# Kernel optimization log

Hardware: AMD Instinct MI355X
Metric: run time of the kernel (lower is better)

The kernel has to match this reference:

```python
import jax, jax.numpy as jnp
import numpy as np

EMBED_DIM = 1024
NUM_HEADS = 16
HEAD_DIM = EMBED_DIM // NUM_HEADS


def setup_inputs() -> dict:
    key = jax.random.key(0)
    k1, k2, k3 = jax.random.split(key, 3)
    B, S = 2, 2048
    scale_in = 1.0 / np.sqrt(EMBED_DIM)
    x = jax.random.normal(k1, (B, S, EMBED_DIM), dtype=jnp.float32)
    Wqkv = jax.random.normal(k2, (EMBED_DIM, 3 * EMBED_DIM), dtype=jnp.float32) * scale_in
    bqkv = jnp.zeros((3 * EMBED_DIM,), dtype=jnp.float32)
    Wout = jax.random.normal(k3, (EMBED_DIM, EMBED_DIM), dtype=jnp.float32) * scale_in
    bout = jnp.zeros((EMBED_DIM,), dtype=jnp.float32)
    return {"x": x, "Wqkv": Wqkv, "bqkv": bqkv, "Wout": Wout, "bout": bout}


def reference(x, Wqkv, bqkv, Wout, bout):
    # Causal multi-head self-attention (dropout in eval mode = identity).
    B, S, E = x.shape
    qkv = x @ Wqkv + bqkv                                  # [B,S,3E]
    qkv = qkv.reshape(B, S, 3, NUM_HEADS, HEAD_DIM)
    qkv = jnp.transpose(qkv, (2, 0, 3, 1, 4))              # [3,B,H,S,D]
    q, k, v = qkv[0], qkv[1], qkv[2]
    scores = jnp.einsum("bhqd,bhkd->bhqk", q, k) / np.sqrt(HEAD_DIM)
    causal = jnp.tril(jnp.ones((S, S), dtype=bool))
    scores = jnp.where(causal, scores, -jnp.inf)
    attn = jax.nn.softmax(scores, axis=-1)                 # [B,H,S,S]
    out = jnp.einsum("bhqk,bhkd->bhqd", attn, v)           # [B,H,S,D]
    out = jnp.transpose(out, (0, 2, 1, 3)).reshape(B, S, E)
    return out @ Wout + bout
```

## Files before the change

kernel.cpp:

```cpp
#include <hip/hip_runtime.h>
#include <hip/hip_bf16.h>

#define BB 2
#define SS 2048
#define EE 1024
#define HH 16
#define DD 64
#define MT (BB*SS)
#define NQ (3*EE)

typedef unsigned short u16;
typedef __bf16 bf16t;
typedef bf16t bf16x8 __attribute__((ext_vector_type(8)));
typedef short short8v __attribute__((ext_vector_type(8)));
typedef float f32x4 __attribute__((ext_vector_type(4)));

#define AS1 __attribute__((address_space(1)))
#define AS3 __attribute__((address_space(3)))

__device__ __forceinline__ u16 f2b(float f) {
  unsigned u = __builtin_bit_cast(unsigned, f);
  u += 0x7FFF + ((u >> 16) & 1);
  return (u16)(u >> 16);
}

__device__ __forceinline__ unsigned cvtpk(float lo, float hi) {
  unsigned r;
  asm("v_cvt_pk_bf16_f32 %0, %1, %2" : "=v"(r) : "v"(lo), "v"(hi));
  return r;
}

__device__ __forceinline__ void gload_lds16(const void* g, void* l) {
  __builtin_amdgcn_global_load_lds((const AS1 void*)(g), (AS3 void*)(l), 16, 0, 0);
}

__device__ __forceinline__ f32x4 mfma_bf16(short8v a, short8v b, f32x4 c) {
  return __builtin_amdgcn_mfma_f32_16x16x32_bf16(
      __builtin_bit_cast(bf16x8, a), __builtin_bit_cast(bf16x8, b), c, 0, 0, 0);
}

#define QSCALE 0.18033688f

__global__ void __launch_bounds__(256) cast_kernel(const float* __restrict__ in,
                                                   u16* __restrict__ out, int n) {
  int i = (blockIdx.x * 256 + threadIdx.x) * 4;
  if (i + 3 < n) {
    float4 v = *(const float4*)(in + i);
    ushort4 o;
    o.x = f2b(v.x); o.y = f2b(v.y); o.z = f2b(v.z); o.w = f2b(v.w);
    *(ushort4*)(out + i) = o;
  }
}

__global__ void __launch_bounds__(256) transpose_kernel(const float* __restrict__ W,
                                                        u16* __restrict__ WT,
                                                        int K, int N) {
  __shared__ float t[64][65];
  int k0 = blockIdx.y * 64, n0 = blockIdx.x * 64;
  int r = threadIdx.x >> 4;
  int c4 = (threadIdx.x & 15) * 4;
#pragma unroll
  for (int i = 0; i < 4; ++i) {
    float4 v = *(const float4*)(W + (size_t)(k0 + r + i * 16) * N + n0 + c4);
    t[r + i * 16][c4 + 0] = v.x; t[r + i * 16][c4 + 1] = v.y;
    t[r + i * 16][c4 + 2] = v.z; t[r + i * 16][c4 + 3] = v.w;
  }
  __syncthreads();
#pragma unroll
  for (int i = 0; i < 4; ++i) {
    ushort4 o;
    o.x = f2b(t[c4 + 0][r + i * 16]); o.y = f2b(t[c4 + 1][r + i * 16]);
    o.z = f2b(t[c4 + 2][r + i * 16]); o.w = f2b(t[c4 + 3][r + i * 16]);
    *(ushort4*)(WT + (size_t)(n0 + r + i * 16) * K + k0 + c4) = o;
  }
}

__global__ void __launch_bounds__(256) gemm_qkv_kernel(
    const u16* __restrict__ A, const u16* __restrict__ BT,
    const float* __restrict__ bias,
    u16* __restrict__ Qs, u16* __restrict__ Ks, u16* __restrict__ Vt) {
  __shared__ u16 As[8192];
  __shared__ u16 Bs[8192];
  const int K = EE;
  int tid = threadIdx.x;
  int w = tid >> 6, lane = tid & 63;
  int g = lane >> 4, q = lane & 15;
  int m0 = blockIdx.y * 128, n0 = blockIdx.x * 128;
  int wm = (w >> 1) * 64, wn = (w & 1) * 64;

  f32x4 acc[4][4] = {};

  int r = tid >> 2;
  int kc = (tid & 3) * 8;
  const u16* ga = A + (size_t)(m0 + r) * K + kc;
  const u16* gb = BT + (size_t)(n0 + r) * K + kc;
  u16* lA0 = As + w * 512;
  u16* lA1 = As + 2048 + w * 512;
  u16* lB0 = Bs + w * 512;
  u16* lB1 = Bs + 2048 + w * 512;

  gload_lds16(ga, lA0);
  gload_lds16(ga + 64 * K, lA1);
  gload_lds16(gb, lB0);
  gload_lds16(gb + 64 * K, lB1);
  ga += 32; gb += 32;
  __syncthreads();

  int cur = 0;
  for (int k0 = 0; k0 < K; k0 += 32) {
    if (k0 + 32 < K) {
      int nx = (cur ^ 1) * 4096;
      gload_lds16(ga, lA0 + nx);
      gload_lds16(ga + 64 * K, lA1 + nx);
      gload_lds16(gb, lB0 + nx);
      gload_lds16(gb + 64 * K, lB1 + nx);
      ga += 32; gb += 32;
    }
    const u16* Ab = As + cur * 4096;
    const u16* Bb = Bs + cur * 4096;
    short8v af[4], bfv[4];
#pragma unroll
    for (int m = 0; m < 4; ++m)
      af[m] = *(const short8v*)(Ab + (wm + m * 16 + q) * 32 + g * 8);
#pragma unroll
    for (int n = 0; n < 4; ++n)
      bfv[n] = *(const short8v*)(Bb + (wn + n * 16 + q) * 32 + g * 8);
#pragma unroll
    for (int m = 0; m < 4; ++m)
#pragma unroll
      for (int n = 0; n < 4; ++n)
        acc[m][n] = mfma_bf16(af[m], bfv[n], acc[m][n]);
    __syncthreads();
    cur ^= 1;
  }

#pragma unroll
  for (int m = 0; m < 4; ++m) {
    int row0 = m0 + wm + m * 16 + g * 4;
#pragma unroll
    for (int n = 0; n < 4; ++n) {
      int col = n0 + wn + n * 16 + q;
      float bi = bias[col];
      int t = col >> 10;
      int h = (col >> 6) & 15;
      int d = col & 63;
      int b = row0 >> 11, s0 = row0 & 2047;
      size_t bh = (size_t)b * HH + h;
      if (t == 2) {
        ushort4 vv;
        vv.x = f2b(acc[m][n][0] + bi); vv.y = f2b(acc[m][n][1] + bi);
        vv.z = f2b(acc[m][n][2] + bi); vv.w = f2b(acc[m][n][3] + bi);
        *(ushort4*)&Vt[(bh * DD + d) * SS + s0] = vv;
      } else if (t == 0) {
#pragma unroll
        for (int r2 = 0; r2 < 4; ++r2)
          Qs[(bh * SS + s0 + r2) * DD + d] = f2b((acc[m][n][r2] + bi) * QSCALE);
      } else {
#pragma unroll
        for (int r2 = 0; r2 < 4; ++r2)
          Ks[(bh * SS + s0 + r2) * DD + d] = f2b(acc[m][n][r2] + bi);
      }
    }
  }
}

__global__ void __launch_bounds__(512) attn_kernel(
    const u16* __restrict__ Qg, const u16* __restrict__ Kg,
    const u16* __restrict__ Vg, u16* __restrict__ O) {
  __shared__ char lds[49152];
  const int tid = threadIdx.x;
  const int w = tid >> 6, lane = tid & 63;
  const int g = lane >> 4, q = lane & 15;
  const int bid = blockIdx.x;
  const int bh = bid & 31;
  const int p = 15 - (bid >> 5);
  const int b = bh >> 4, h = bh & 15;
  char* Pw = lds + 32768 + w * 2048;
  const int qsw = (q & 7) << 4;

  const char* Qp = (const char*)Qg + (size_t)bh * (SS * 128);
  const char* Kp = (const char*)Kg + (size_t)bh * (SS * 128);
  const char* Vp = (const char*)Vg + (size_t)bh * (SS * 128);

  const int srow = tid >> 3;
  const int ssw = ((tid & 7) * 16) ^ ((srow & 7) << 4);
  const char* Ksrc = Kp + srow * 128 + ssw;
  const char* Vsrc = Vp + (size_t)srow * (SS * 2) + ssw;
  char* Kdst = lds + w * 1024;
  char* Vdst = lds + 16384 + w * 1024;

  const int nt = 2 * p + 2;
  const int qw = p * 128 + w * 16;

  short8v aq0 = *(const short8v*)(Qp + (size_t)(qw + q) * 128 + g * 16);
  short8v aq1 = *(const short8v*)(Qp + (size_t)(qw + q) * 128 + 64 + g * 16);

  f32x4 oacc[4] = {};
  float mrun = -1e30f, lrun = 0.f;

  gload_lds16(Ksrc, Kdst);
  gload_lds16(Vsrc, Vdst);
  __syncthreads();

  for (int s = 0; s < nt; ++s) {
    const int buf = s & 1;
    if (s + 1 < nt) {
      gload_lds16(Ksrc + (size_t)(s + 1) * 8192, Kdst + (buf ^ 1) * 8192);
      gload_lds16(Vsrc + (s + 1) * 128, Vdst + (buf ^ 1) * 8192);
    }
    const int kv0 = s << 6;
    if (kv0 <= qw + 15) {
      const char* Kc = lds + buf * 8192;
      const char* Vc = lds + 16384 + buf * 8192;
      short8v kf[4][2];
#pragma unroll
      for (int cc = 0; cc < 4; ++cc) {
        const char* kb = Kc + (cc * 16 + q) * 128;
        kf[cc][0] = *(const short8v*)(kb + ((g * 16) ^ qsw));
        kf[cc][1] = *(const short8v*)(kb + ((64 + g * 16) ^ qsw));
      }
      f32x4 st[4];
#pragma unroll
      for (int cc = 0; cc < 4; ++cc) {
        f32x4 z = {};
        z = mfma_bf16(kf[cc][0], aq0, z);
        z = mfma_bf16(kf[cc][1], aq1, z);
        st[cc] = z;
      }
      short8v vf[4][2];
#pragma unroll
      for (int v = 0; v < 4; ++v) {
        const char* vb = Vc + (v * 16 + q) * 128;
        vf[v][0] = *(const short8v*)(vb + ((g * 16) ^ qsw));
        vf[v][1] = *(const short8v*)(vb + ((64 + g * 16) ^ qsw));
      }
      if (kv0 + 63 > qw) {
        int row = qw + q;
#pragma unroll
        for (int cc = 0; cc < 4; ++cc) {
          int kvb = kv0 + cc * 16 + g * 4;
#pragma unroll
          for (int r2 = 0; r2 < 4; ++r2)
            if (kvb + r2 > row) st[cc][r2] = -1e30f;
        }
      }
      f32x4 t01, t23;
#pragma unroll
      for (int r2 = 0; r2 < 4; ++r2) {
        t01[r2] = fmaxf(st[0][r2], st[1][r2]);
        t23[r2] = fmaxf(st[2][r2], st[3][r2]);
      }
      float mx = fmaxf(fmaxf(fmaxf(t01[0], t01[1]), fmaxf(t01[2], t01[3])),
                       fmaxf(fmaxf(t23[0], t23[1]), fmaxf(t23[2], t23[3])));
      mx = fmaxf(mx, __shfl_xor(mx, 16));
      mx = fmaxf(mx, __shfl_xor(mx, 32));
      if (!__all(mx - mrun <= 8.f)) {
        float mnew = fmaxf(mrun, mx);
        float alpha = exp2f(mrun - mnew);
        mrun = mnew;
        lrun *= alpha;
#pragma unroll
        for (int vfi = 0; vfi < 4; ++vfi)
#pragma unroll
          for (int r2 = 0; r2 < 4; ++r2) oacc[vfi][r2] *= alpha;
      }
      f32x4 sum4 = {};
#pragma unroll
      for (int cc = 0; cc < 4; ++cc)
#pragma unroll
        for (int r2 = 0; r2 < 4; ++r2) {
          float pv = exp2f(st[cc][r2] - mrun);
          st[cc][r2] = pv;
          sum4[r2] += pv;
        }
      float sm = (sum4[0] + sum4[1]) + (sum4[2] + sum4[3]);
      sm += __shfl_xor(sm, 16);
      sm += __shfl_xor(sm, 32);
      lrun += sm;
      char* basep = Pw + q * 128;
#pragma unroll
      for (int cc = 0; cc < 4; ++cc) {
        unsigned p01 = cvtpk(st[cc][0], st[cc][1]);
        unsigned p23 = cvtpk(st[cc][2], st[cc][3]);
        *(unsigned*)(basep + ((32 * cc + 8 * g + 0) ^ qsw)) = p01;
        *(unsigned*)(basep + ((32 * cc + 8 * g + 4) ^ qsw)) = p23;
      }
      short8v pa0 = *(const short8v*)(basep + ((g * 16) ^ qsw));
      short8v pa1 = *(const short8v*)(basep + ((64 + g * 16) ^ qsw));
#pragma unroll
      for (int vfi = 0; vfi < 4; ++vfi) {
        oacc[vfi] = mfma_bf16(vf[vfi][0], pa0, oacc[vfi]);
        oacc[vfi] = mfma_bf16(vf[vfi][1], pa1, oacc[vfi]);
      }
    }
    __syncthreads();
  }

  {
    float inv = 1.0f / lrun;
    int row = qw + q;
    char* obase = (char*)O + (((size_t)b * SS + row) * EE + h * 64) * 2;
#pragma unroll
    for (int vfi = 0; vfi < 4; ++vfi) {
      uint2 o;
      o.x = cvtpk(oacc[vfi][0] * inv, oacc[vfi][1] * inv);
      o.y = cvtpk(oacc[vfi][2] * inv, oacc[vfi][3] * inv);
      *(uint2*)(obase + (vfi * 16 + g * 4) * 2) = o;
    }
  }
}

__global__ void __launch_bounds__(256) gemm_out_kernel(
    const u16* __restrict__ A, const u16* __restrict__ BT,
    const float* __restrict__ bias, float* __restrict__ Cout) {
  __shared__ u16 As[8192];
  __shared__ u16 Bs[8192];
  const int K = EE;
  int tid = threadIdx.x;
  int w = tid >> 6, lane = tid & 63;
  int g = lane >> 4, q = lane & 15;
  int m0 = blockIdx.y * 128, n0 = blockIdx.x * 128;
  int wm = (w >> 1) * 64, wn = (w & 1) * 64;

  f32x4 acc[4][4] = {};

  int r = tid >> 2;
  int kc = (tid & 3) * 8;
  const u16* ga = A + (size_t)(m0 + r) * K + kc;
  const u16* gb = BT + (size_t)(n0 + r) * K + kc;
  u16* lA0 = As + w * 512;
  u16* lA1 = As + 2048 + w * 512;
  u16* lB0 = Bs + w * 512;
  u16* lB1 = Bs + 2048 + w * 512;

  gload_lds16(ga, lA0);
  gload_lds16(ga + 64 * K, lA1);
  gload_lds16(gb, lB0);
  gload_lds16(gb + 64 * K, lB1);
  ga += 32; gb += 32;
  __syncthreads();

  int cur = 0;
  for (int k0 = 0; k0 < K; k0 += 32) {
    if (k0 + 32 < K) {
      int nx = (cur ^ 1) * 4096;
      gload_lds16(ga, lA0 + nx);
      gload_lds16(ga + 64 * K, lA1 + nx);
      gload_lds16(gb, lB0 + nx);
      gload_lds16(gb + 64 * K, lB1 + nx);
      ga += 32; gb += 32;
    }
    const u16* Ab = As + cur * 4096;
    const u16* Bb = Bs + cur * 4096;
    short8v af[4], bfv[4];
#pragma unroll
    for (int m = 0; m < 4; ++m)
      af[m] = *(const short8v*)(Ab + (wm + m * 16 + q) * 32 + g * 8);
#pragma unroll
    for (int n = 0; n < 4; ++n)
      bfv[n] = *(const short8v*)(Bb + (wn + n * 16 + q) * 32 + g * 8);
#pragma unroll
    for (int m = 0; m < 4; ++m)
#pragma unroll
      for (int n = 0; n < 4; ++n)
        acc[m][n] = mfma_bf16(af[m], bfv[n], acc[m][n]);
    __syncthreads();
    cur ^= 1;
  }

#pragma unroll
  for (int m = 0; m < 4; ++m) {
    int row0 = m0 + wm + m * 16 + g * 4;
#pragma unroll
    for (int n = 0; n < 4; ++n) {
      int col = n0 + wn + n * 16 + q;
      float bi = bias[col];
#pragma unroll
      for (int r2 = 0; r2 < 4; ++r2) {
        int row = row0 + r2;
        Cout[(size_t)row * EE + col] = acc[m][n][r2] + bi;
      }
    }
  }
}

extern "C" void kernel_launch(void* const* d_in, const int* in_sizes, int n_in,
                              void* d_out, int out_size, void* d_ws, size_t ws_size,
                              hipStream_t stream) {
  (void)in_sizes; (void)n_in; (void)out_size; (void)ws_size;
  const float* x    = (const float*)d_in[0];
  const float* Wqkv = (const float*)d_in[1];
  const float* bqkv = (const float*)d_in[2];
  const float* Wout = (const float*)d_in[3];
  const float* bout = (const float*)d_in[4];
  float* out = (float*)d_out;

  char* p = (char*)d_ws;
  u16* xb  = (u16*)p; p += (size_t)MT * EE * 2;
  u16* wqT = (u16*)p; p += (size_t)NQ * EE * 2;
  u16* woT = (u16*)p; p += (size_t)EE * EE * 2;
  u16* Qs  = (u16*)p; p += (size_t)BB * HH * SS * DD * 2;
  u16* Ks  = (u16*)p; p += (size_t)BB * HH * SS * DD * 2;
  u16* Vt  = (u16*)p; p += (size_t)BB * HH * DD * SS * 2;
  u16* Ob  = (u16*)p; p += (size_t)MT * EE * 2;

  cast_kernel<<<dim3((MT * EE / 4) / 256), dim3(256), 0, stream>>>(x, xb, MT * EE);
  transpose_kernel<<<dim3(NQ / 64, EE / 64), dim3(256), 0, stream>>>(Wqkv, wqT, EE, NQ);
  transpose_kernel<<<dim3(EE / 64, EE / 64), dim3(256), 0, stream>>>(Wout, woT, EE, EE);
  gemm_qkv_kernel<<<dim3(NQ / 128, MT / 128), dim3(256), 0, stream>>>(xb, wqT, bqkv, Qs, Ks, Vt);
  attn_kernel<<<dim3(512), dim3(512), 0, stream>>>(Qs, Ks, Vt, Ob);
  gemm_out_kernel<<<dim3(EE / 128, MT / 128), dim3(256), 0, stream>>>(Ob, woT, bout, out);
}
```

Baseline: 121.1 us.

## Split attention into 64-row query blocks with snake ordering and MFMA priority

The attention kernel moves from 512 blocks of 8 waves (128 query rows each) to 1024 blocks of 4 waves (64 query rows each). Each thread now issues two K and two V LDS loads per tile to fill the same 64-row tile, and LDS shrinks to 40 KB. Causal blocks are ordered in a serpentine pattern so consecutive blocks get balanced work. s_setprio brackets around the MFMA loops raise wave priority during matrix ops. The intent is better occupancy and load balance across CUs, at the cost of more blocks each reloading K/V with less reuse per block.

Result: slower. 126.5 us (+4.5%).

```diff
diff --git a/kernel.cpp b/kernel.cpp
--- a/kernel.cpp
+++ b/kernel.cpp
@@ -164,16 +164,18 @@
   }
 }
 
-__global__ void __launch_bounds__(512) attn_kernel(
+__global__ void __launch_bounds__(256) attn_kernel(
     const u16* __restrict__ Qg, const u16* __restrict__ Kg,
     const u16* __restrict__ Vg, u16* __restrict__ O) {
-  __shared__ char lds[49152];
+  __shared__ char lds[40960];
   const int tid = threadIdx.x;
   const int w = tid >> 6, lane = tid & 63;
   const int g = lane >> 4, q = lane & 15;
   const int bid = blockIdx.x;
   const int bh = bid & 31;
-  const int p = 15 - (bid >> 5);
+  const int i = bid >> 5;
+  const int t8 = i >> 3, r8 = i & 7;
+  const int c = (t8 & 1) ? (8 * t8 + 7 - r8) : (8 * t8 + r8);
   const int b = bh >> 4, h = bh & 15;
   char* Pw = lds + 32768 + w * 2048;
   const int qsw = (q & 7) << 4;
@@ -182,15 +184,21 @@
   const char* Kp = (const char*)Kg + (size_t)bh * (SS * 128);
   const char* Vp = (const char*)Vg + (size_t)bh * (SS * 128);
 
-  const int srow = tid >> 3;
-  const int ssw = ((tid & 7) * 16) ^ ((srow & 7) << 4);
-  const char* Ksrc = Kp + srow * 128 + ssw;
-  const char* Vsrc = Vp + (size_t)srow * (SS * 2) + ssw;
-  char* Kdst = lds + w * 1024;
-  char* Vdst = lds + 16384 + w * 1024;
-
-  const int nt = 2 * p + 2;
-  const int qw = p * 128 + w * 16;
+  const int sr0 = tid >> 3;
+  const int sc0 = ((tid & 7) * 16) ^ ((sr0 & 7) << 4);
+  const int sr1 = (tid + 256) >> 3;
+  const int sc1 = ((tid & 7) * 16) ^ ((sr1 & 7) << 4);
+  const char* Ksrc0 = Kp + sr0 * 128 + sc0;
+  const char* Ksrc1 = Kp + sr1 * 128 + sc1;
+  const char* Vsrc0 = Vp + (size_t)sr0 * (SS * 2) + sc0;
+  const char* Vsrc1 = Vp + (size_t)sr1 * (SS * 2) + sc1;
+  char* Kd0 = lds + w * 1024;
+  char* Kd1 = lds + w * 1024 + 4096;
+  char* Vd0 = lds + 16384 + w * 1024;
+  char* Vd1 = lds + 16384 + w * 1024 + 4096;
+
+  const int nt = c + 1;
+  const int qw = c * 64 + w * 16;
 
   short8v aq0 = *(const short8v*)(Qp + (size_t)(qw + q) * 128 + g * 16);
   short8v aq1 = *(const short8v*)(Qp + (size_t)(qw + q) * 128 + 64 + g * 16);
@@ -198,15 +206,22 @@
   f32x4 oacc[4] = {};
   float mrun = -1e30f, lrun = 0.f;
 
-  gload_lds16(Ksrc, Kdst);
-  gload_lds16(Vsrc, Vdst);
+  gload_lds16(Ksrc0, Kd0);
+  gload_lds16(Ksrc1, Kd1);
+  gload_lds16(Vsrc0, Vd0);
+  gload_lds16(Vsrc1, Vd1);
   __syncthreads();
 
   for (int s = 0; s < nt; ++s) {
     const int buf = s & 1;
     if (s + 1 < nt) {
-      gload_lds16(Ksrc + (size_t)(s + 1) * 8192, Kdst + (buf ^ 1) * 8192);
-      gload_lds16(Vsrc + (s + 1) * 128, Vdst + (buf ^ 1) * 8192);
+      size_t ko = (size_t)(s + 1) * 8192;
+      int vo = (s + 1) * 128;
+      int bo = (buf ^ 1) * 8192;
+      gload_lds16(Ksrc0 + ko, Kd0 + bo);
+      gload_lds16(Ksrc1 + ko, Kd1 + bo);
+      gload_lds16(Vsrc0 + vo, Vd0 + bo);
+      gload_lds16(Vsrc1 + vo, Vd1 + bo);
     }
     const int kv0 = s << 6;
     if (kv0 <= qw + 15) {
@@ -220,6 +235,7 @@
         kf[cc][1] = *(const short8v*)(kb + ((64 + g * 16) ^ qsw));
       }
       f32x4 st[4];
+      __builtin_amdgcn_s_setprio(1);
 #pragma unroll
       for (int cc = 0; cc < 4; ++cc) {
         f32x4 z = {};
@@ -227,6 +243,7 @@
         z = mfma_bf16(kf[cc][1], aq1, z);
         st[cc] = z;
       }
+      __builtin_amdgcn_s_setprio(0);
       short8v vf[4][2];
 #pragma unroll
       for (int v = 0; v < 4; ++v) {
@@ -287,11 +304,13 @@
       }
       short8v pa0 = *(const short8v*)(basep + ((g * 16) ^ qsw));
       short8v pa1 = *(const short8v*)(basep + ((64 + g * 16) ^ qsw));
+      __builtin_amdgcn_s_setprio(1);
 #pragma unroll
       for (int vfi = 0; vfi < 4; ++vfi) {
         oacc[vfi] = mfma_bf16(vf[vfi][0], pa0, oacc[vfi]);
         oacc[vfi] = mfma_bf16(vf[vfi][1], pa1, oacc[vfi]);
       }
+      __builtin_amdgcn_s_setprio(0);
     }
     __syncthreads();
   }
@@ -408,6 +427,6 @@
   transpose_kernel<<<dim3(NQ / 64, EE / 64), dim3(256), 0, stream>>>(Wqkv, wqT, EE, NQ);
   transpose_kernel<<<dim3(EE / 64, EE / 64), dim3(256), 0, stream>>>(Wout, woT, EE, EE);
   gemm_qkv_kernel<<<dim3(NQ / 128, MT / 128), dim3(256), 0, stream>>>(xb, wqT, bqkv, Qs, Ks, Vt);
-  attn_kernel<<<dim3(512), dim3(512), 0, stream>>>(Qs, Ks, Vt, Ob);
+  attn_kernel<<<dim3(1024), dim3(256), 0, stream>>>(Qs, Ks, Vt, Ob);
   gemm_out_kernel<<<dim3(EE / 128, MT / 128), dim3(256), 0, stream>>>(Ob, woT, bout, out);
 }
```

## Process 128-key KV tiles per iteration with one softmax rescale per tile

Applied to the files above, without the earlier changes.

The attention loop now stages 128 keys of K and V per stage instead of 64, doubling the LDS buffers, and processes the tile as two 64-key halves. It computes one row max and one rescale across both halves and reduces the row sum once. This halves the number of barriers, prefetch rounds and max/shuffle reductions per query block. The cost is more LDS per block (80 KB), which can lower occupancy, and coarser causal skipping because only the second half can be skipped.

Result: no change. 121.1 us (-0.0%).

```diff
diff --git a/kernel.cpp b/kernel.cpp
--- a/kernel.cpp
+++ b/kernel.cpp
@@ -167,7 +167,7 @@
 __global__ void __launch_bounds__(512) attn_kernel(
     const u16* __restrict__ Qg, const u16* __restrict__ Kg,
     const u16* __restrict__ Vg, u16* __restrict__ O) {
-  __shared__ char lds[49152];
+  __shared__ char lds[81920];
   const int tid = threadIdx.x;
   const int w = tid >> 6, lane = tid & 63;
   const int g = lane >> 4, q = lane & 15;
@@ -175,21 +175,31 @@
   const int bh = bid & 31;
   const int p = 15 - (bid >> 5);
   const int b = bh >> 4, h = bh & 15;
-  char* Pw = lds + 32768 + w * 2048;
+  char* Pw = lds + 65536 + w * 2048;
   const int qsw = (q & 7) << 4;
 
   const char* Qp = (const char*)Qg + (size_t)bh * (SS * 128);
   const char* Kp = (const char*)Kg + (size_t)bh * (SS * 128);
   const char* Vp = (const char*)Vg + (size_t)bh * (SS * 128);
 
-  const int srow = tid >> 3;
-  const int ssw = ((tid & 7) * 16) ^ ((srow & 7) << 4);
-  const char* Ksrc = Kp + srow * 128 + ssw;
-  const char* Vsrc = Vp + (size_t)srow * (SS * 2) + ssw;
-  char* Kdst = lds + w * 1024;
-  char* Vdst = lds + 16384 + w * 1024;
-
-  const int nt = 2 * p + 2;
+  const int kr0 = tid >> 3;
+  const int kc0 = ((tid & 7) * 16) ^ ((kr0 & 7) << 4);
+  const int kr1 = (tid + 512) >> 3;
+  const int kc1 = ((tid & 7) * 16) ^ ((kr1 & 7) << 4);
+  const char* Ksrc0 = Kp + kr0 * 128 + kc0;
+  const char* Ksrc1 = Kp + kr1 * 128 + kc1;
+  const int vr0 = tid >> 4, vh0 = (tid & 15) >> 3;
+  const int vc0 = vh0 * 128 + ((((tid & 7)) * 16) ^ ((vr0 & 7) << 4));
+  const int vr1 = (tid + 512) >> 4, vh1 = ((tid + 512) & 15) >> 3;
+  const int vc1 = vh1 * 128 + ((((tid & 7)) * 16) ^ ((vr1 & 7) << 4));
+  const char* Vsrc0 = Vp + (size_t)vr0 * (SS * 2) + vc0;
+  const char* Vsrc1 = Vp + (size_t)vr1 * (SS * 2) + vc1;
+  char* Kd0 = lds + w * 1024;
+  char* Kd1 = lds + 8192 + w * 1024;
+  char* Vd0 = lds + 32768 + w * 1024;
+  char* Vd1 = lds + 32768 + 8192 + w * 1024;
+
+  const int np = p + 1;
   const int qw = p * 128 + w * 16;
 
   short8v aq0 = *(const short8v*)(Qp + (size_t)(qw + q) * 128 + g * 16);
@@ -198,20 +208,30 @@
   f32x4 oacc[4] = {};
   float mrun = -1e30f, lrun = 0.f;
 
-  gload_lds16(Ksrc, Kdst);
-  gload_lds16(Vsrc, Vdst);
+  gload_lds16(Ksrc0, Kd0);
+  gload_lds16(Ksrc1, Kd1);
+  gload_lds16(Vsrc0, Vd0);
+  gload_lds16(Vsrc1, Vd1);
   __syncthreads();
 
-  for (int s = 0; s < nt; ++s) {
-    const int buf = s & 1;
-    if (s + 1 < nt) {
-      gload_lds16(Ksrc + (size_t)(s + 1) * 8192, Kdst + (buf ^ 1) * 8192);
-      gload_lds16(Vsrc + (s + 1) * 128, Vdst + (buf ^ 1) * 8192);
-    }
-    const int kv0 = s << 6;
-    if (kv0 <= qw + 15) {
-      const char* Kc = lds + buf * 8192;
-      const char* Vc = lds + 16384 + buf * 8192;
+  for (int ph = 0; ph < np; ++ph) {
+    const int buf = ph & 1;
+    if (ph + 1 < np) {
+      size_t ko = (size_t)(ph + 1) * 16384;
+      int vo = (ph + 1) * 256;
+      int bo = (buf ^ 1) * 16384;
+      gload_lds16(Ksrc0 + ko, Kd0 + bo);
+      gload_lds16(Ksrc1 + ko, Kd1 + bo);
+      gload_lds16(Vsrc0 + vo, Vd0 + bo);
+      gload_lds16(Vsrc1 + vo, Vd1 + bo);
+    }
+    const int kv0 = ph << 7;
+    const char* Kc = lds + buf * 16384;
+    const char* Vc = lds + 32768 + buf * 16384;
+    const bool actB = (kv0 + 64) <= qw + 15;
+
+    f32x4 stA[4], stB[4];
+    {
       short8v kf[4][2];
 #pragma unroll
       for (int cc = 0; cc < 4; ++cc) {
@@ -219,69 +239,95 @@
         kf[cc][0] = *(const short8v*)(kb + ((g * 16) ^ qsw));
         kf[cc][1] = *(const short8v*)(kb + ((64 + g * 16) ^ qsw));
       }
-      f32x4 st[4];
 #pragma unroll
       for (int cc = 0; cc < 4; ++cc) {
         f32x4 z = {};
         z = mfma_bf16(kf[cc][0], aq0, z);
         z = mfma_bf16(kf[cc][1], aq1, z);
-        st[cc] = z;
-      }
-      short8v vf[4][2];
-#pragma unroll
-      for (int v = 0; v < 4; ++v) {
-        const char* vb = Vc + (v * 16 + q) * 128;
-        vf[v][0] = *(const short8v*)(vb + ((g * 16) ^ qsw));
-        vf[v][1] = *(const short8v*)(vb + ((64 + g * 16) ^ qsw));
-      }
-      if (kv0 + 63 > qw) {
-        int row = qw + q;
+        stA[cc] = z;
+      }
+    }
+    if (actB) {
+      short8v kf[4][2];
+#pragma unroll
+      for (int cc = 0; cc < 4; ++cc) {
+        const char* kb = Kc + (64 + cc * 16 + q) * 128;
+        kf[cc][0] = *(const short8v*)(kb + ((g * 16) ^ qsw));
+        kf[cc][1] = *(const short8v*)(kb + ((64 + g * 16) ^ qsw));
+      }
+#pragma unroll
+      for (int cc = 0; cc < 4; ++cc) {
+        f32x4 z = {};
+        z = mfma_bf16(kf[cc][0], aq0, z);
+        z = mfma_bf16(kf[cc][1], aq1, z);
+        stB[cc] = z;
+      }
+    }
+    {
+      int row = qw + q;
+      if (kv0 + 63 > row - 15) {
 #pragma unroll
         for (int cc = 0; cc < 4; ++cc) {
           int kvb = kv0 + cc * 16 + g * 4;
 #pragma unroll
           for (int r2 = 0; r2 < 4; ++r2)
-            if (kvb + r2 > row) st[cc][r2] = -1e30f;
+            if (kvb + r2 > row) stA[cc][r2] = -1e30f;
         }
       }
-      f32x4 t01, t23;
+      if (actB && kv0 + 127 > row - 15) {
+#pragma unroll
+        for (int cc = 0; cc < 4; ++cc) {
+          int kvb = kv0 + 64 + cc * 16 + g * 4;
+#pragma unroll
+          for (int r2 = 0; r2 < 4; ++r2)
+            if (kvb + r2 > row) stB[cc][r2] = -1e30f;
+        }
+      }
+    }
+    f32x4 t01, t23;
+#pragma unroll
+    for (int r2 = 0; r2 < 4; ++r2) {
+      t01[r2] = fmaxf(stA[0][r2], stA[1][r2]);
+      t23[r2] = fmaxf(stA[2][r2], stA[3][r2]);
+    }
+    if (actB) {
 #pragma unroll
       for (int r2 = 0; r2 < 4; ++r2) {
-        t01[r2] = fmaxf(st[0][r2], st[1][r2]);
-        t23[r2] = fmaxf(st[2][r2], st[3][r2]);
-      }
-      float mx = fmaxf(fmaxf(fmaxf(t01[0], t01[1]), fmaxf(t01[2], t01[3])),
-                       fmaxf(fmaxf(t23[0], t23[1]), fmaxf(t23[2], t23[3])));
-      mx = fmaxf(mx, __shfl_xor(mx, 16));
-      mx = fmaxf(mx, __shfl_xor(mx, 32));
-      if (!__all(mx - mrun <= 8.f)) {
-        float mnew = fmaxf(mrun, mx);
-        float alpha = exp2f(mrun - mnew);
-        mrun = mnew;
-        lrun *= alpha;
-#pragma unroll
-        for (int vfi = 0; vfi < 4; ++vfi)
-#pragma unroll
-          for (int r2 = 0; r2 < 4; ++r2) oacc[vfi][r2] *= alpha;
-      }
+        t01[r2] = fmaxf(t01[r2], fmaxf(stB[0][r2], stB[1][r2]));
+        t23[r2] = fmaxf(t23[r2], fmaxf(stB[2][r2], stB[3][r2]));
+      }
+    }
+    float mx = fmaxf(fmaxf(fmaxf(t01[0], t01[1]), fmaxf(t01[2], t01[3])),
+                     fmaxf(fmaxf(t23[0], t23[1]), fmaxf(t23[2], t23[3])));
+    mx = fmaxf(mx, __shfl_xor(mx, 16));
+    mx = fmaxf(mx, __shfl_xor(mx, 32));
+    if (!__all(mx - mrun <= 8.f)) {
+      float mnew = fmaxf(mrun, mx);
+      float alpha = exp2f(mrun - mnew);
+      mrun = mnew;
+      lrun *= alpha;
+#pragma unroll
+      for (int vfi = 0; vfi < 4; ++vfi)
+#pragma unroll
+        for (int r2 = 0; r2 < 4; ++r2) oacc[vfi][r2] *= alpha;
+    }
+    float sml;
+    {
       f32x4 sum4 = {};
 #pragma unroll
       for (int cc = 0; cc < 4; ++cc)
 #pragma unroll
         for (int r2 = 0; r2 < 4; ++r2) {
-          float pv = exp2f(st[cc][r2] - mrun);
-          st[cc][r2] = pv;
+          float pv = exp2f(stA[cc][r2] - mrun);
+          stA[cc][r2] = pv;
           sum4[r2] += pv;
         }
-      float sm = (sum4[0] + sum4[1]) + (sum4[2] + sum4[3]);
-      sm += __shfl_xor(sm, 16);
-      sm += __shfl_xor(sm, 32);
-      lrun += sm;
+      sml = (sum4[0] + sum4[1]) + (sum4[2] + sum4[3]);
       char* basep = Pw + q * 128;
 #pragma unroll
       for (int cc = 0; cc < 4; ++cc) {
-        unsigned p01 = cvtpk(st[cc][0], st[cc][1]);
-        unsigned p23 = cvtpk(st[cc][2], st[cc][3]);
+        unsigned p01 = cvtpk(stA[cc][0], stA[cc][1]);
+        unsigned p23 = cvtpk(stA[cc][2], stA[cc][3]);
         *(unsigned*)(basep + ((32 * cc + 8 * g + 0) ^ qsw)) = p01;
         *(unsigned*)(basep + ((32 * cc + 8 * g + 4) ^ qsw)) = p23;
       }
@@ -289,10 +335,46 @@
       short8v pa1 = *(const short8v*)(basep + ((64 + g * 16) ^ qsw));
 #pragma unroll
       for (int vfi = 0; vfi < 4; ++vfi) {
-        oacc[vfi] = mfma_bf16(vf[vfi][0], pa0, oacc[vfi]);
-        oacc[vfi] = mfma_bf16(vf[vfi][1], pa1, oacc[vfi]);
-      }
-    }
+        const char* vb = Vc + (vfi * 16 + q) * 256;
+        short8v v0 = *(const short8v*)(vb + ((g * 16) ^ qsw));
+        short8v v1 = *(const short8v*)(vb + ((64 + g * 16) ^ qsw));
+        oacc[vfi] = mfma_bf16(v0, pa0, oacc[vfi]);
+        oacc[vfi] = mfma_bf16(v1, pa1, oacc[vfi]);
+      }
+    }
+    if (actB) {
+      f32x4 sum4 = {};
+#pragma unroll
+      for (int cc = 0; cc < 4; ++cc)
+#pragma unroll
+        for (int r2 = 0; r2 < 4; ++r2) {
+          float pv = exp2f(stB[cc][r2] - mrun);
+          stB[cc][r2] = pv;
+          sum4[r2] += pv;
+        }
+      sml += (sum4[0] + sum4[1]) + (sum4[2] + sum4[3]);
+      char* basep = Pw + q * 128;
+#pragma unroll
+      for (int cc = 0; cc < 4; ++cc) {
+        unsigned p01 = cvtpk(stB[cc][0], stB[cc][1]);
+        unsigned p23 = cvtpk(stB[cc][2], stB[cc][3]);
+        *(unsigned*)(basep + ((32 * cc + 8 * g + 0) ^ qsw)) = p01;
+        *(unsigned*)(basep + ((32 * cc + 8 * g + 4) ^ qsw)) = p23;
+      }
+      short8v pa0 = *(const short8v*)(basep + ((g * 16) ^ qsw));
+      short8v pa1 = *(const short8v*)(basep + ((64 + g * 16) ^ qsw));
+#pragma unroll
+      for (int vfi = 0; vfi < 4; ++vfi) {
+        const char* vb = Vc + (vfi * 16 + q) * 256 + 128;
+        short8v v0 = *(const short8v*)(vb + ((g * 16) ^ qsw));
+        short8v v1 = *(const short8v*)(vb + ((64 + g * 16) ^ qsw));
+        oacc[vfi] = mfma_bf16(v0, pa0, oacc[vfi]);
+        oacc[vfi] = mfma_bf16(v1, pa1, oacc[vfi]);
+      }
+    }
+    sml += __shfl_xor(sml, 16);
+    sml += __shfl_xor(sml, 32);
+    lrun += sml;
     __syncthreads();
   }
 
```

## Split attention KV range across two wave halves with triple-buffered loads and merge

Applied to the files above, without the earlier changes.

Doubles the attention block to 1024 threads. The two halves of 8 waves each process half of the causal KV tiles for the same 128 query rows, and their partial softmax states (max, sum, output accumulator) are merged through LDS at the end. The K/V staging moves from double buffering with a full __syncthreads to triple buffering, using explicit vmcnt waits and raw s_barrier so loads run two tiles ahead. This aims to shorten the serial KV loop for long causal rows and to hide more load latency. In exchange it raises LDS use to about 129 KB per block, which limits occupancy to one block per CU, and it adds a merge step.

New measurement: 117.0 us. 3.3% less time.

```diff
diff --git a/kernel.cpp b/kernel.cpp
--- a/kernel.cpp
+++ b/kernel.cpp
@@ -164,33 +164,36 @@
   }
 }
 
-__global__ void __launch_bounds__(512) attn_kernel(
+__global__ void __launch_bounds__(1024) attn_kernel(
     const u16* __restrict__ Qg, const u16* __restrict__ Kg,
     const u16* __restrict__ Vg, u16* __restrict__ O) {
-  __shared__ char lds[49152];
+  __shared__ char lds[132096];
   const int tid = threadIdx.x;
   const int w = tid >> 6, lane = tid & 63;
+  const int hv = w >> 3, ws = w & 7;
   const int g = lane >> 4, q = lane & 15;
   const int bid = blockIdx.x;
   const int bh = bid & 31;
   const int p = 15 - (bid >> 5);
   const int b = bh >> 4, h = bh & 15;
-  char* Pw = lds + 32768 + w * 2048;
+  char* Pw = lds + 98304 + w * 2048;
   const int qsw = (q & 7) << 4;
 
   const char* Qp = (const char*)Qg + (size_t)bh * (SS * 128);
   const char* Kp = (const char*)Kg + (size_t)bh * (SS * 128);
   const char* Vp = (const char*)Vg + (size_t)bh * (SS * 128);
 
-  const int srow = tid >> 3;
-  const int ssw = ((tid & 7) * 16) ^ ((srow & 7) << 4);
+  const int tl = tid & 511;
+  const int srow = tl >> 3;
+  const int ssw = ((tl & 7) * 16) ^ ((srow & 7) << 4);
   const char* Ksrc = Kp + srow * 128 + ssw;
   const char* Vsrc = Vp + (size_t)srow * (SS * 2) + ssw;
-  char* Kdst = lds + w * 1024;
-  char* Vdst = lds + 16384 + w * 1024;
-
-  const int nt = 2 * p + 2;
-  const int qw = p * 128 + w * 16;
+  char* Kdst = lds + hv * 24576 + ws * 1024;
+  char* Vdst = lds + 49152 + hv * 24576 + ws * 1024;
+
+  const int hl = p + 1;
+  const int s0 = hv * hl, send = s0 + hl;
+  const int qw = p * 128 + ws * 16;
 
   short8v aq0 = *(const short8v*)(Qp + (size_t)(qw + q) * 128 + g * 16);
   short8v aq1 = *(const short8v*)(Qp + (size_t)(qw + q) * 128 + 64 + g * 16);
@@ -198,20 +201,27 @@
   f32x4 oacc[4] = {};
   float mrun = -1e30f, lrun = 0.f;
 
-  gload_lds16(Ksrc, Kdst);
-  gload_lds16(Vsrc, Vdst);
-  __syncthreads();
-
-  for (int s = 0; s < nt; ++s) {
-    const int buf = s & 1;
-    if (s + 1 < nt) {
-      gload_lds16(Ksrc + (size_t)(s + 1) * 8192, Kdst + (buf ^ 1) * 8192);
-      gload_lds16(Vsrc + (s + 1) * 128, Vdst + (buf ^ 1) * 8192);
+  gload_lds16(Ksrc + (size_t)s0 * 8192, Kdst);
+  gload_lds16(Vsrc + s0 * 128, Vdst);
+  if (hl > 1) {
+    gload_lds16(Ksrc + (size_t)(s0 + 1) * 8192, Kdst + 8192);
+    gload_lds16(Vsrc + (s0 + 1) * 128, Vdst + 8192);
+  }
+
+  for (int s = s0; s < send; ++s) {
+    const int buf = (s - s0) % 3;
+    if (s + 1 < send) asm volatile("s_waitcnt vmcnt(2)" ::: "memory");
+    else              asm volatile("s_waitcnt vmcnt(0)" ::: "memory");
+    __builtin_amdgcn_s_barrier();
+    if (s + 2 < send) {
+      int nb = (s + 2 - s0) % 3;
+      gload_lds16(Ksrc + (size_t)(s + 2) * 8192, Kdst + nb * 8192);
+      gload_lds16(Vsrc + (s + 2) * 128, Vdst + nb * 8192);
     }
     const int kv0 = s << 6;
     if (kv0 <= qw + 15) {
-      const char* Kc = lds + buf * 8192;
-      const char* Vc = lds + 16384 + buf * 8192;
+      const char* Kc = lds + hv * 24576 + buf * 8192;
+      const char* Vc = lds + 49152 + hv * 24576 + buf * 8192;
       short8v kf[4][2];
 #pragma unroll
       for (int cc = 0; cc < 4; ++cc) {
@@ -293,18 +303,36 @@
         oacc[vfi] = mfma_bf16(vf[vfi][1], pa1, oacc[vfi]);
       }
     }
-    __syncthreads();
-  }
-
-  {
-    float inv = 1.0f / lrun;
+  }
+
+  __syncthreads();
+  if (hv) {
+    char* ob = lds + 98304 + ws * 4096;
+#pragma unroll
+    for (int vfi = 0; vfi < 4; ++vfi)
+      *(f32x4*)(ob + vfi * 1024 + lane * 16) = oacc[vfi];
+    if (g == 0)
+      *(float2*)(lds + 131072 + (ws * 16 + q) * 8) = make_float2(mrun, lrun);
+  }
+  __syncthreads();
+  if (!hv) {
+    float2 ml = *(const float2*)(lds + 131072 + (ws * 16 + q) * 8);
+    float mf = fmaxf(mrun, ml.x);
+    float a0 = exp2f(mrun - mf);
+    float a1 = exp2f(ml.x - mf);
+    float inv = 1.0f / (a0 * lrun + a1 * ml.y);
+    a0 *= inv; a1 *= inv;
+    const char* ob = lds + 98304 + ws * 4096;
     int row = qw + q;
     char* obase = (char*)O + (((size_t)b * SS + row) * EE + h * 64) * 2;
 #pragma unroll
     for (int vfi = 0; vfi < 4; ++vfi) {
+      f32x4 o1 = *(const f32x4*)(ob + vfi * 1024 + lane * 16);
       uint2 o;
-      o.x = cvtpk(oacc[vfi][0] * inv, oacc[vfi][1] * inv);
-      o.y = cvtpk(oacc[vfi][2] * inv, oacc[vfi][3] * inv);
+      o.x = cvtpk(a0 * oacc[vfi][0] + a1 * o1[0],
+                  a0 * oacc[vfi][1] + a1 * o1[1]);
+      o.y = cvtpk(a0 * oacc[vfi][2] + a1 * o1[2],
+                  a0 * oacc[vfi][3] + a1 * o1[3]);
       *(uint2*)(obase + (vfi * 16 + g * 4) * 2) = o;
     }
   }
@@ -408,6 +436,6 @@
   transpose_kernel<<<dim3(NQ / 64, EE / 64), dim3(256), 0, stream>>>(Wqkv, wqT, EE, NQ);
   transpose_kernel<<<dim3(EE / 64, EE / 64), dim3(256), 0, stream>>>(Wout, woT, EE, EE);
   gemm_qkv_kernel<<<dim3(NQ / 128, MT / 128), dim3(256), 0, stream>>>(xb, wqT, bqkv, Qs, Ks, Vt);
-  attn_kernel<<<dim3(512), dim3(512), 0, stream>>>(Qs, Ks, Vt, Ob);
+  attn_kernel<<<dim3(512), dim3(1024), 0, stream>>>(Qs, Ks, Vt, Ob);
   gemm_out_kernel<<<dim3(EE / 128, MT / 128), dim3(256), 0, stream>>>(Ob, woT, bout, out);
 }
```
